# Kernel tuning notes

Hardware: AMD Instinct MI355X
Metric: run time of the kernel (lower is better)

Reference implementation:

```python
import jax, jax.numpy as jnp
import numpy as np

EMBED_DIM = 1024
TASK_BIAS_DIM = 128
BATCH = 4
SEQ = 2048


def setup_inputs() -> dict:
    key = jax.random.key(0)
    kq, kk, kv, kt, kw, kb = jax.random.split(key, 6)
    query = jax.random.normal(kq, (BATCH, SEQ, EMBED_DIM), dtype=jnp.float32)
    key_t = jax.random.normal(kk, (BATCH, SEQ, EMBED_DIM), dtype=jnp.float32)
    value = jax.random.normal(kv, (BATCH, SEQ, EMBED_DIM), dtype=jnp.float32)
    task_bias = jax.random.normal(kt, (BATCH, TASK_BIAS_DIM), dtype=jnp.float32)
    # task_bias_proj: Linear(task_bias_dim, 1) -> weight [1, task_bias_dim], bias [1]
    lim = 1.0 / np.sqrt(TASK_BIAS_DIM)
    W = jax.random.uniform(kw, (TASK_BIAS_DIM, 1), jnp.float32, -lim, lim)
    b = jax.random.uniform(kb, (1,), jnp.float32, -lim, lim)
    return {"query": query, "key": key_t, "value": value,
            "task_bias": task_bias, "W": W, "b": b}


def reference(query, key, value, task_bias, W, b):
    scale = EMBED_DIM ** 0.5
    # scores: [batch, seq, seq]
    scores = jnp.einsum('bqd,bkd->bqk', query, key) / scale
    # per-batch scalar gate from task bias: [batch, 1]
    gate = jax.nn.sigmoid(task_bias @ W + b)           # [batch, 1]
    scores = scores * gate[:, :, None]                 # broadcast [b,1,1]
    attention_weights = jax.nn.softmax(scores, axis=-1)
    output = jnp.einsum('bqk,bkd->bqd', attention_weights, value)
    return output, attention_weights
```

## Files before the change

kernel.cpp:

```cpp
#include <hip/hip_runtime.h>
#include <hip/hip_bf16.h>
#include <stdint.h>
#include <stddef.h>

#define B_  4
#define S_  2048
#define D_  1024
#define TB_ 128

typedef float v4f  __attribute__((ext_vector_type(4)));
typedef float v16f __attribute__((ext_vector_type(16)));
typedef short s16x4 __attribute__((ext_vector_type(4)));
typedef short s16x8 __attribute__((ext_vector_type(8)));

#define WAITV(n) asm volatile("s_waitcnt vmcnt(" #n ")" ::: "memory")

__device__ __forceinline__ unsigned short f2bf(float f) {
  union { float f; unsigned u; } x; x.f = f;
  unsigned u = x.u;
  unsigned r = (u + 0x7FFFu + ((u >> 16) & 1u)) >> 16;
  return (unsigned short)r;
}

__device__ __forceinline__ void gld16(const void* g, void* l) {
  __builtin_amdgcn_global_load_lds(
      (const __attribute__((address_space(1))) unsigned int*)g,
      (__attribute__((address_space(3))) unsigned int*)l, 16, 0, 0);
}

__device__ __forceinline__ void barrier_sync() {
  asm volatile("" ::: "memory");
  __builtin_amdgcn_s_barrier();
  asm volatile("" ::: "memory");
  __builtin_amdgcn_sched_barrier(0);
}

__global__ __launch_bounds__(256) void prep_kernel(
    const float* __restrict__ Q, const float* __restrict__ K,
    const float* __restrict__ V, const float* __restrict__ tb,
    const float* __restrict__ W, const float* __restrict__ bias,
    short* __restrict__ Qb, short* __restrict__ Kb,
    short* __restrict__ VT, float* __restrict__ gate) {
  __shared__ float tile[64][65];
  int bid = blockIdx.x;
  int t = threadIdx.x;
  if (bid < 16384) {
    const float* src = bid < 8192 ? Q : K;
    short* dst = bid < 8192 ? Qb : Kb;
    size_t g = (size_t)(bid & 8191) * 256 + t;
    v4f v = *(const v4f*)(src + g * 4);
    s16x4 o;
    o[0] = (short)f2bf(v[0]); o[1] = (short)f2bf(v[1]);
    o[2] = (short)f2bf(v[2]); o[3] = (short)f2bf(v[3]);
    *(s16x4*)(dst + g * 4) = o;
  } else if (bid < 18432) {
    int v = bid - 16384;
    int b = v >> 9;
    int rem = v & 511;
    int s0 = (rem & 31) * 64, d0 = (rem >> 5) * 64;
    int tc = t & 63, tr4 = t >> 6;
    const float* src = V + ((size_t)b * S_ + s0) * D_ + d0;
    #pragma unroll
    for (int p = 0; p < 16; ++p) {
      int r = p * 4 + tr4;
      tile[r][tc] = src[(size_t)r * D_ + tc];
    }
    __syncthreads();
    short* dst = VT + ((size_t)b * D_ + d0) * S_ + s0;
    #pragma unroll
    for (int p = 0; p < 16; ++p) {
      int r = p * 4 + tr4;
      dst[(size_t)r * S_ + tc] = (short)f2bf(tile[tc][r]);
    }
  } else {
    int b = t >> 6, l = t & 63;
    float s = tb[b * TB_ + l] * W[l] + tb[b * TB_ + 64 + l] * W[64 + l];
    #pragma unroll
    for (int off = 32; off > 0; off >>= 1) s += __shfl_down(s, off, 64);
    if (l == 0) gate[b] = 1.0f / (1.0f + __expf(-(s + bias[0])));
  }
}

template<int MFR, int NFR, int WNC, int BLOADS, int KT, int BROWS, int LDC,
         bool GATED>
__global__ __launch_bounds__(512, 2) void gemm_pipe(
    const short* __restrict__ Ag, const short* __restrict__ Bg,
    const float* __restrict__ gate, float* __restrict__ Cg) {
  extern __shared__ char lds[];
  constexpr int NT = KT / 64;
  constexpr int BN = WNC * NFR * 32;
  constexpr int ABYTES = 256 * 128;
  constexpr int BBYTES = BN * 128;
  constexpr int BUFB = ABYTES + BBYTES;

  int wg = blockIdx.x;
  int swz = (wg & 7) * 32 + (wg >> 3);
  int b = swz >> 6;
  int rem = swz & 63;
  int m0 = (rem >> 3) * 256;
  int n0 = (rem & 7) * BN;

  int tid = threadIdx.x;
  int w = tid >> 6, l = tid & 63;
  int wm = w / WNC, wn = w % WNC;
  int l7 = l & 7, col31 = l & 31, hi2 = l >> 5;

  const short* Ab = Ag + (size_t)b * S_ * KT + (size_t)m0 * KT;
  const short* Bb = Bg + (size_t)b * BROWS * KT + (size_t)n0 * KT;

  int srow8 = l >> 3;
  int schunk = ((l & 7) ^ srow8) * 8;

  v16f acc[MFR][NFR];
  #pragma unroll
  for (int m = 0; m < MFR; ++m)
    #pragma unroll
    for (int n = 0; n < NFR; ++n)
      #pragma unroll
      for (int j = 0; j < 16; ++j) acc[m][n][j] = 0.0f;

  auto stage = [&](int t, int buf) {
    char* La = lds + buf * BUFB;
    char* Lb = La + ABYTES;
    const short* As = Ab + (size_t)t * 64 + schunk;
    #pragma unroll
    for (int j = 0; j < 4; ++j) {
      int blk = w * 4 + j;
      gld16(As + (size_t)(blk * 8 + srow8) * KT, La + blk * 1024);
    }
    const short* Bs = Bb + (size_t)t * 64 + schunk;
    #pragma unroll
    for (int j = 0; j < BLOADS; ++j) {
      int blk = w * BLOADS + j;
      gld16(Bs + (size_t)(blk * 8 + srow8) * KT, Lb + blk * 1024);
    }
  };

  stage(0, 0);
  int cur = 0;
  for (int t = 0; t < NT; ++t) {
    if (t + 1 < NT) {
      stage(t + 1, cur ^ 1);
      if constexpr (BLOADS == 4) WAITV(8); else WAITV(6);
    } else {
      WAITV(0);
    }
    barrier_sync();
    const char* Abase = lds + cur * BUFB;
    const char* Bbase = Abase + ABYTES;
    #pragma unroll
    for (int ks = 0; ks < 4; ++ks) {
      int slot = ((ks * 2 + hi2) ^ l7) * 16;
      s16x8 bfr[NFR], af[MFR];
      #pragma unroll
      for (int n = 0; n < NFR; ++n)
        bfr[n] = *(const s16x8*)(Bbase +
                 (size_t)(wn * (NFR * 32) + n * 32 + col31) * 128 + slot);
      #pragma unroll
      for (int m = 0; m < MFR; ++m)
        af[m] = *(const s16x8*)(Abase +
                 (size_t)(wm * (MFR * 32) + m * 32 + col31) * 128 + slot);
      __builtin_amdgcn_s_setprio(1);
      #pragma unroll
      for (int m = 0; m < MFR; ++m)
        #pragma unroll
        for (int n = 0; n < NFR; ++n)
          acc[m][n] = __builtin_amdgcn_mfma_f32_32x32x16_bf16(
              af[m], bfr[n], acc[m][n], 0, 0, 0);
      __builtin_amdgcn_s_setprio(0);
    }
    barrier_sync();
    cur ^= 1;
  }

  float g = 1.0f;
  if constexpr (GATED) g = gate[b] * 0.03125f;
  float* Cb = Cg + (size_t)b * S_ * LDC +
              (size_t)(m0 + wm * (MFR * 32)) * LDC + n0 + wn * (NFR * 32);
  #pragma unroll
  for (int mf = 0; mf < MFR; ++mf)
    #pragma unroll
    for (int nf = 0; nf < NFR; ++nf) {
      int c = nf * 32 + col31;
      #pragma unroll
      for (int q = 0; q < 4; ++q)
        #pragma unroll
        for (int j = 0; j < 4; ++j) {
          int r = mf * 32 + q * 8 + 4 * hi2 + j;
          Cb[(size_t)r * LDC + c] = acc[mf][nf][q * 4 + j] * g;
        }
    }
}

__global__ __launch_bounds__(256) void softmax_kernel(
    float* __restrict__ attn, short* __restrict__ attnb) {
  size_t row = blockIdx.x;
  float* p = attn + row * S_;
  int t = threadIdx.x;
  v4f v0 = *(const v4f*)(p + t * 8);
  v4f v1 = *(const v4f*)(p + t * 8 + 4);
  float m = fmaxf(fmaxf(fmaxf(v0[0], v0[1]), fmaxf(v0[2], v0[3])),
                  fmaxf(fmaxf(v1[0], v1[1]), fmaxf(v1[2], v1[3])));
  #pragma unroll
  for (int off = 32; off > 0; off >>= 1) m = fmaxf(m, __shfl_xor(m, off, 64));
  __shared__ float rm[4], rs[4];
  if ((t & 63) == 0) rm[t >> 6] = m;
  __syncthreads();
  m = fmaxf(fmaxf(rm[0], rm[1]), fmaxf(rm[2], rm[3]));
  float e[8]; float sum = 0.0f;
  #pragma unroll
  for (int j = 0; j < 4; ++j) { e[j] = __expf(v0[j] - m); sum += e[j]; }
  #pragma unroll
  for (int j = 0; j < 4; ++j) { e[4 + j] = __expf(v1[j] - m); sum += e[4 + j]; }
  #pragma unroll
  for (int off = 32; off > 0; off >>= 1) sum += __shfl_xor(sum, off, 64);
  if ((t & 63) == 0) rs[t >> 6] = sum;
  __syncthreads();
  sum = rs[0] + rs[1] + rs[2] + rs[3];
  float inv = 1.0f / sum;
  #pragma unroll
  for (int j = 0; j < 4; ++j) v0[j] = e[j] * inv;
  #pragma unroll
  for (int j = 0; j < 4; ++j) v1[j] = e[4 + j] * inv;
  *(v4f*)(p + t * 8) = v0;
  *(v4f*)(p + t * 8 + 4) = v1;
  s16x8 ob;
  ob[0] = (short)f2bf(v0[0]); ob[1] = (short)f2bf(v0[1]);
  ob[2] = (short)f2bf(v0[2]); ob[3] = (short)f2bf(v0[3]);
  ob[4] = (short)f2bf(v1[0]); ob[5] = (short)f2bf(v1[1]);
  ob[6] = (short)f2bf(v1[2]); ob[7] = (short)f2bf(v1[3]);
  *(s16x8*)(attnb + row * S_ + t * 8) = ob;
}

extern "C" void kernel_launch(void* const* d_in, const int* in_sizes, int n_in,
                              void* d_out, int out_size, void* d_ws, size_t ws_size,
                              hipStream_t stream) {
  (void)in_sizes; (void)n_in; (void)out_size; (void)ws_size;
  const float* Q  = (const float*)d_in[0];
  const float* K  = (const float*)d_in[1];
  const float* V  = (const float*)d_in[2];
  const float* tb = (const float*)d_in[3];
  const float* W  = (const float*)d_in[4];
  const float* bias = (const float*)d_in[5];

  float* out  = (float*)d_out;
  float* attn = out + (size_t)B_ * S_ * D_;

  char* ws = (char*)d_ws;
  float* gate = (float*)ws;
  short* Qb = (short*)(ws + 256);
  short* Kb = Qb + (size_t)B_ * S_ * D_;
  short* VT = Kb + (size_t)B_ * S_ * D_;
  short* attnb = Qb;

  auto* qkf = gemm_pipe<4, 2, 4, 4, 1024, 2048, 2048, true>;
  auto* pvf = gemm_pipe<2, 2, 2, 2, 2048, 1024, 1024, false>;
  constexpr int QK_LDS = 2 * (256 + 256) * 64 * 2;
  constexpr int PV_LDS = 2 * (256 + 128) * 64 * 2;
  (void)hipFuncSetAttribute((const void*)qkf,
      hipFuncAttributeMaxDynamicSharedMemorySize, QK_LDS);
  (void)hipFuncSetAttribute((const void*)pvf,
      hipFuncAttributeMaxDynamicSharedMemorySize, PV_LDS);

  prep_kernel<<<18433, 256, 0, stream>>>(Q, K, V, tb, W, bias,
                                         Qb, Kb, VT, gate);
  qkf<<<256, 512, QK_LDS, stream>>>(Qb, Kb, gate, attn);
  softmax_kernel<<<8192, 256, 0, stream>>>(attn, attnb);
  pvf<<<256, 512, PV_LDS, stream>>>(attnb, VT, gate, out);
}
```

Measured before the change: 136.9 us.

## Shrink GEMM tiles to 128x128 with 256-thread blocks for more parallelism

Replaces the large-tile GEMM (256x256 or 256x128 per 512-thread block) with a 128x128 tile per 256-thread block where each wave computes a 64x64 sub-tile. This quadruples the grid for QK^T (1024 blocks) and doubles it for PV (512 blocks), aiming at better CU fill and wave-level parallelism on the 256-CU device. The cost is lower arithmetic intensity per tile: more global/LDS traffic per MFMA and fewer MFMAs per LDS fragment load.

```diff
diff --git a/kernel.cpp b/kernel.cpp
--- a/kernel.cpp
+++ b/kernel.cpp
@@ -81,41 +81,40 @@
   }
 }
 
-template<int MFR, int NFR, int WNC, int BLOADS, int KT, int BROWS, int LDC,
-         bool GATED>
-__global__ __launch_bounds__(512, 2) void gemm_pipe(
+template<int MTILES, int NTILES, int KT, int BROWS, int LDC, bool GATED>
+__global__ __launch_bounds__(256, 2) void gemm_tlp(
     const short* __restrict__ Ag, const short* __restrict__ Bg,
     const float* __restrict__ gate, float* __restrict__ Cg) {
   extern __shared__ char lds[];
   constexpr int NT = KT / 64;
-  constexpr int BN = WNC * NFR * 32;
-  constexpr int ABYTES = 256 * 128;
-  constexpr int BBYTES = BN * 128;
-  constexpr int BUFB = ABYTES + BBYTES;
+  constexpr int PB = MTILES * NTILES;
+  constexpr int CPX = (4 * PB) / 8;
+  constexpr int ABYTES = 128 * 128;
+  constexpr int BUFB = 2 * ABYTES;
 
   int wg = blockIdx.x;
-  int swz = (wg & 7) * 32 + (wg >> 3);
-  int b = swz >> 6;
-  int rem = swz & 63;
-  int m0 = (rem >> 3) * 256;
-  int n0 = (rem & 7) * BN;
+  int swz = (wg & 7) * CPX + (wg >> 3);
+  int b = swz / PB;
+  int rem = swz % PB;
+  int m0 = (rem / NTILES) * 128;
+  int n0 = (rem % NTILES) * 128;
 
   int tid = threadIdx.x;
   int w = tid >> 6, l = tid & 63;
-  int wm = w / WNC, wn = w % WNC;
+  int wm = w >> 1, wn = w & 1;
   int l7 = l & 7, col31 = l & 31, hi2 = l >> 5;
 
   const short* Ab = Ag + (size_t)b * S_ * KT + (size_t)m0 * KT;
   const short* Bb = Bg + (size_t)b * BROWS * KT + (size_t)n0 * KT;
 
-  int srow8 = l >> 3;
-  int schunk = ((l & 7) ^ srow8) * 8;
-
-  v16f acc[MFR][NFR];
-  #pragma unroll
-  for (int m = 0; m < MFR; ++m)
-    #pragma unroll
-    for (int n = 0; n < NFR; ++n)
+  int srow = tid >> 3;
+  int schunk = ((tid & 7) ^ (srow & 7)) * 8;
+
+  v16f acc[2][2];
+  #pragma unroll
+  for (int m = 0; m < 2; ++m)
+    #pragma unroll
+    for (int n = 0; n < 2; ++n)
       #pragma unroll
       for (int j = 0; j < 16; ++j) acc[m][n][j] = 0.0f;
 
@@ -123,17 +122,13 @@
     char* La = lds + buf * BUFB;
     char* Lb = La + ABYTES;
     const short* As = Ab + (size_t)t * 64 + schunk;
-    #pragma unroll
-    for (int j = 0; j < 4; ++j) {
-      int blk = w * 4 + j;
-      gld16(As + (size_t)(blk * 8 + srow8) * KT, La + blk * 1024);
-    }
     const short* Bs = Bb + (size_t)t * 64 + schunk;
     #pragma unroll
-    for (int j = 0; j < BLOADS; ++j) {
-      int blk = w * BLOADS + j;
-      gld16(Bs + (size_t)(blk * 8 + srow8) * KT, Lb + blk * 1024);
-    }
+    for (int j = 0; j < 4; ++j)
+      gld16(As + (size_t)(j * 32 + srow) * KT, La + j * 4096 + tid * 16);
+    #pragma unroll
+    for (int j = 0; j < 4; ++j)
+      gld16(Bs + (size_t)(j * 32 + srow) * KT, Lb + j * 4096 + tid * 16);
   };
 
   stage(0, 0);
@@ -141,7 +136,7 @@
   for (int t = 0; t < NT; ++t) {
     if (t + 1 < NT) {
       stage(t + 1, cur ^ 1);
-      if constexpr (BLOADS == 4) WAITV(8); else WAITV(6);
+      WAITV(8);
     } else {
       WAITV(0);
     }
@@ -151,20 +146,20 @@
     #pragma unroll
     for (int ks = 0; ks < 4; ++ks) {
       int slot = ((ks * 2 + hi2) ^ l7) * 16;
-      s16x8 bfr[NFR], af[MFR];
-      #pragma unroll
-      for (int n = 0; n < NFR; ++n)
+      s16x8 af[2], bfr[2];
+      #pragma unroll
+      for (int m = 0; m < 2; ++m)
+        af[m] = *(const s16x8*)(Abase +
+                 (size_t)(wm * 64 + m * 32 + col31) * 128 + slot);
+      #pragma unroll
+      for (int n = 0; n < 2; ++n)
         bfr[n] = *(const s16x8*)(Bbase +
-                 (size_t)(wn * (NFR * 32) + n * 32 + col31) * 128 + slot);
-      #pragma unroll
-      for (int m = 0; m < MFR; ++m)
-        af[m] = *(const s16x8*)(Abase +
-                 (size_t)(wm * (MFR * 32) + m * 32 + col31) * 128 + slot);
+                 (size_t)(wn * 64 + n * 32 + col31) * 128 + slot);
       __builtin_amdgcn_s_setprio(1);
       #pragma unroll
-      for (int m = 0; m < MFR; ++m)
+      for (int m = 0; m < 2; ++m)
         #pragma unroll
-        for (int n = 0; n < NFR; ++n)
+        for (int n = 0; n < 2; ++n)
           acc[m][n] = __builtin_amdgcn_mfma_f32_32x32x16_bf16(
               af[m], bfr[n], acc[m][n], 0, 0, 0);
       __builtin_amdgcn_s_setprio(0);
@@ -176,11 +171,11 @@
   float g = 1.0f;
   if constexpr (GATED) g = gate[b] * 0.03125f;
   float* Cb = Cg + (size_t)b * S_ * LDC +
-              (size_t)(m0 + wm * (MFR * 32)) * LDC + n0 + wn * (NFR * 32);
-  #pragma unroll
-  for (int mf = 0; mf < MFR; ++mf)
-    #pragma unroll
-    for (int nf = 0; nf < NFR; ++nf) {
+              (size_t)(m0 + wm * 64) * LDC + n0 + wn * 64;
+  #pragma unroll
+  for (int mf = 0; mf < 2; ++mf)
+    #pragma unroll
+    for (int nf = 0; nf < 2; ++nf) {
       int c = nf * 32 + col31;
       #pragma unroll
       for (int q = 0; q < 4; ++q)
@@ -253,18 +248,17 @@
   short* VT = Kb + (size_t)B_ * S_ * D_;
   short* attnb = Qb;
 
-  auto* qkf = gemm_pipe<4, 2, 4, 4, 1024, 2048, 2048, true>;
-  auto* pvf = gemm_pipe<2, 2, 2, 2, 2048, 1024, 1024, false>;
-  constexpr int QK_LDS = 2 * (256 + 256) * 64 * 2;
-  constexpr int PV_LDS = 2 * (256 + 128) * 64 * 2;
+  auto* qkf = gemm_tlp<16, 16, 1024, 2048, 2048, true>;
+  auto* pvf = gemm_tlp<16, 8, 2048, 1024, 1024, false>;
+  constexpr int G_LDS = 65536;
   (void)hipFuncSetAttribute((const void*)qkf,
-      hipFuncAttributeMaxDynamicSharedMemorySize, QK_LDS);
+      hipFuncAttributeMaxDynamicSharedMemorySize, G_LDS);
   (void)hipFuncSetAttribute((const void*)pvf,
-      hipFuncAttributeMaxDynamicSharedMemorySize, PV_LDS);
+      hipFuncAttributeMaxDynamicSharedMemorySize, G_LDS);
 
   prep_kernel<<<18433, 256, 0, stream>>>(Q, K, V, tb, W, bias,
                                          Qb, Kb, VT, gate);
-  qkf<<<256, 512, QK_LDS, stream>>>(Qb, Kb, gate, attn);
+  qkf<<<1024, 256, G_LDS, stream>>>(Qb, Kb, gate, attn);
   softmax_kernel<<<8192, 256, 0, stream>>>(attn, attnb);
-  pvf<<<256, 512, PV_LDS, stream>>>(attnb, VT, gate, out);
-}
+  pvf<<<512, 256, G_LDS, stream>>>(attnb, VT, gate, out);
+}
```

Result: slower. 141.7 us (+3.4%).

## Shrink GEMM workgroups and K-step to raise occupancy and workgroup count

Applied to the files above, without the earlier changes.

Restructures the bf16 MFMA GEMM kernel. Workgroups drop from 512 to 256 threads (4 waves in a 2x2 grid), output tiles shrink (256x128 for QK, 128x128 for PV), and the K-step per pipeline stage halves from 64 to 32 with a matching 4-chunk LDS swizzle. The grid doubles to 512 blocks and LDS per block drops, so more blocks can be resident per CU and the 256 CUs get more even coverage. The cost is more K iterations with a barrier each, less data reuse per tile, and more global traffic relative to the MFMA work.

```diff
diff --git a/kernel.cpp b/kernel.cpp
--- a/kernel.cpp
+++ b/kernel.cpp
@@ -81,35 +81,39 @@
   }
 }
 
-template<int MFR, int NFR, int WNC, int BLOADS, int KT, int BROWS, int LDC,
-         bool GATED>
-__global__ __launch_bounds__(512, 2) void gemm_pipe(
+template<int MTILES, int NTILES, int MFR, int NFR, int KT, int BROWS,
+         int LDC, bool GATED>
+__global__ __launch_bounds__(256, 2) void gemm_occ(
     const short* __restrict__ Ag, const short* __restrict__ Bg,
     const float* __restrict__ gate, float* __restrict__ Cg) {
   extern __shared__ char lds[];
-  constexpr int NT = KT / 64;
-  constexpr int BN = WNC * NFR * 32;
-  constexpr int ABYTES = 256 * 128;
-  constexpr int BBYTES = BN * 128;
-  constexpr int BUFB = ABYTES + BBYTES;
+  constexpr int BM = MFR * 64;
+  constexpr int BN = NFR * 64;
+  constexpr int ALOADS = BM / 64;
+  constexpr int BLOADS = BN / 64;
+  constexpr int NT = KT / 32;
+  constexpr int PB = MTILES * NTILES;
+  constexpr int CPX = (4 * PB) / 8;
+  constexpr int ABYTES = BM * 64;
+  constexpr int BUFB = ABYTES + BN * 64;
 
   int wg = blockIdx.x;
-  int swz = (wg & 7) * 32 + (wg >> 3);
-  int b = swz >> 6;
-  int rem = swz & 63;
-  int m0 = (rem >> 3) * 256;
-  int n0 = (rem & 7) * BN;
+  int swz = (wg & 7) * CPX + (wg >> 3);
+  int b = swz / PB;
+  int rem = swz % PB;
+  int m0 = (rem / NTILES) * BM;
+  int n0 = (rem % NTILES) * BN;
 
   int tid = threadIdx.x;
   int w = tid >> 6, l = tid & 63;
-  int wm = w / WNC, wn = w % WNC;
-  int l7 = l & 7, col31 = l & 31, hi2 = l >> 5;
+  int wm = w >> 1, wn = w & 1;
+  int col31 = l & 31, hi2 = l >> 5;
 
   const short* Ab = Ag + (size_t)b * S_ * KT + (size_t)m0 * KT;
   const short* Bb = Bg + (size_t)b * BROWS * KT + (size_t)n0 * KT;
 
-  int srow8 = l >> 3;
-  int schunk = ((l & 7) ^ srow8) * 8;
+  int srow = tid >> 2;
+  int schunk = ((tid & 3) ^ (srow & 3)) * 8;
 
   v16f acc[MFR][NFR];
   #pragma unroll
@@ -122,18 +126,14 @@
   auto stage = [&](int t, int buf) {
     char* La = lds + buf * BUFB;
     char* Lb = La + ABYTES;
-    const short* As = Ab + (size_t)t * 64 + schunk;
-    #pragma unroll
-    for (int j = 0; j < 4; ++j) {
-      int blk = w * 4 + j;
-      gld16(As + (size_t)(blk * 8 + srow8) * KT, La + blk * 1024);
-    }
-    const short* Bs = Bb + (size_t)t * 64 + schunk;
-    #pragma unroll
-    for (int j = 0; j < BLOADS; ++j) {
-      int blk = w * BLOADS + j;
-      gld16(Bs + (size_t)(blk * 8 + srow8) * KT, Lb + blk * 1024);
-    }
+    const short* As = Ab + (size_t)t * 32 + schunk;
+    const short* Bs = Bb + (size_t)t * 32 + schunk;
+    #pragma unroll
+    for (int j = 0; j < ALOADS; ++j)
+      gld16(As + (size_t)(j * 64 + srow) * KT, La + j * 4096 + tid * 16);
+    #pragma unroll
+    for (int j = 0; j < BLOADS; ++j)
+      gld16(Bs + (size_t)(j * 64 + srow) * KT, Lb + j * 4096 + tid * 16);
   };
 
   stage(0, 0);
@@ -141,7 +141,7 @@
   for (int t = 0; t < NT; ++t) {
     if (t + 1 < NT) {
       stage(t + 1, cur ^ 1);
-      if constexpr (BLOADS == 4) WAITV(8); else WAITV(6);
+      if constexpr (ALOADS + BLOADS == 6) WAITV(6); else WAITV(4);
     } else {
       WAITV(0);
     }
@@ -149,17 +149,17 @@
     const char* Abase = lds + cur * BUFB;
     const char* Bbase = Abase + ABYTES;
     #pragma unroll
-    for (int ks = 0; ks < 4; ++ks) {
-      int slot = ((ks * 2 + hi2) ^ l7) * 16;
-      s16x8 bfr[NFR], af[MFR];
+    for (int ks = 0; ks < 2; ++ks) {
+      int slot = ((ks * 2 + hi2) ^ (col31 & 3)) * 16;
+      s16x8 af[MFR], bfr[NFR];
+      #pragma unroll
+      for (int m = 0; m < MFR; ++m)
+        af[m] = *(const s16x8*)(Abase +
+                 (size_t)(wm * (MFR * 32) + m * 32 + col31) * 64 + slot);
       #pragma unroll
       for (int n = 0; n < NFR; ++n)
         bfr[n] = *(const s16x8*)(Bbase +
-                 (size_t)(wn * (NFR * 32) + n * 32 + col31) * 128 + slot);
-      #pragma unroll
-      for (int m = 0; m < MFR; ++m)
-        af[m] = *(const s16x8*)(Abase +
-                 (size_t)(wm * (MFR * 32) + m * 32 + col31) * 128 + slot);
+                 (size_t)(wn * (NFR * 32) + n * 32 + col31) * 64 + slot);
       __builtin_amdgcn_s_setprio(1);
       #pragma unroll
       for (int m = 0; m < MFR; ++m)
@@ -253,10 +253,10 @@
   short* VT = Kb + (size_t)B_ * S_ * D_;
   short* attnb = Qb;
 
-  auto* qkf = gemm_pipe<4, 2, 4, 4, 1024, 2048, 2048, true>;
-  auto* pvf = gemm_pipe<2, 2, 2, 2, 2048, 1024, 1024, false>;
-  constexpr int QK_LDS = 2 * (256 + 256) * 64 * 2;
-  constexpr int PV_LDS = 2 * (256 + 128) * 64 * 2;
+  auto* qkf = gemm_occ<8, 16, 4, 2, 1024, 2048, 2048, true>;
+  auto* pvf = gemm_occ<16, 8, 2, 2, 2048, 1024, 1024, false>;
+  constexpr int QK_LDS = 2 * (256 + 128) * 32 * 2;
+  constexpr int PV_LDS = 2 * (128 + 128) * 32 * 2;
   (void)hipFuncSetAttribute((const void*)qkf,
       hipFuncAttributeMaxDynamicSharedMemorySize, QK_LDS);
   (void)hipFuncSetAttribute((const void*)pvf,
@@ -264,7 +264,7 @@
 
   prep_kernel<<<18433, 256, 0, stream>>>(Q, K, V, tb, W, bias,
                                          Qb, Kb, VT, gate);
-  qkf<<<256, 512, QK_LDS, stream>>>(Qb, Kb, gate, attn);
+  qkf<<<512, 256, QK_LDS, stream>>>(Qb, Kb, gate, attn);
   softmax_kernel<<<8192, 256, 0, stream>>>(attn, attnb);
-  pvf<<<256, 512, PV_LDS, stream>>>(attnb, VT, gate, out);
-}
+  pvf<<<512, 256, PV_LDS, stream>>>(attnb, VT, gate, out);
+}
```

Result: slower. 146.7 us (+7.2%).

## Move fp32 attention-weight write from softmax into the PV GEMM epilogue

Applied to the files above, without the earlier changes.

The softmax kernel now writes only the bf16 probabilities. The PV GEMM kernel gains an epilogue in which each block converts 32 rows of the bf16 probabilities back to fp32 and writes them into the attention-weights output. The aim is to shorten the softmax pass and overlap the large fp32 store with the GEMM tail. In exchange, the returned attention weights are rounded to bf16 precision, and total memory traffic grows by an extra read of the bf16 matrix.

```diff
diff --git a/kernel.cpp b/kernel.cpp
--- a/kernel.cpp
+++ b/kernel.cpp
@@ -20,6 +20,12 @@
   unsigned u = x.u;
   unsigned r = (u + 0x7FFFu + ((u >> 16) & 1u)) >> 16;
   return (unsigned short)r;
+}
+
+__device__ __forceinline__ float bf2f(unsigned short s) {
+  union { unsigned u; float f; } x;
+  x.u = (unsigned)s << 16;
+  return x.f;
 }
 
 __device__ __forceinline__ void gld16(const void* g, void* l) {
@@ -82,10 +88,11 @@
 }
 
 template<int MFR, int NFR, int WNC, int BLOADS, int KT, int BROWS, int LDC,
-         bool GATED>
+         bool GATED, bool WATT>
 __global__ __launch_bounds__(512, 2) void gemm_pipe(
     const short* __restrict__ Ag, const short* __restrict__ Bg,
-    const float* __restrict__ gate, float* __restrict__ Cg) {
+    const float* __restrict__ gate, float* __restrict__ Cg,
+    const short* __restrict__ Pfull, float* __restrict__ attnOut) {
   extern __shared__ char lds[];
   constexpr int NT = KT / 64;
   constexpr int BN = WNC * NFR * 32;
@@ -109,7 +116,7 @@
   const short* Bb = Bg + (size_t)b * BROWS * KT + (size_t)n0 * KT;
 
   int srow8 = l >> 3;
-  int schunk = ((l & 7) ^ srow8) * 8;
+  int schunk = (l7 ^ srow8) * 8;
 
   v16f acc[MFR][NFR];
   #pragma unroll
@@ -190,12 +197,29 @@
           Cb[(size_t)r * LDC + c] = acc[mf][nf][q * 4 + j] * g;
         }
     }
+
+  if constexpr (WATT) {
+    int ni = rem & 7;
+    const short* Pb = Pfull + (size_t)b * S_ * S_;
+    float* Ob = attnOut + (size_t)b * S_ * S_;
+    #pragma unroll 4
+    for (int r = 0; r < 32; ++r) {
+      size_t off = (size_t)(m0 + ni * 32 + r) * S_ + tid * 4;
+      s16x4 pv = *(const s16x4*)(Pb + off);
+      v4f o;
+      o[0] = bf2f((unsigned short)pv[0]);
+      o[1] = bf2f((unsigned short)pv[1]);
+      o[2] = bf2f((unsigned short)pv[2]);
+      o[3] = bf2f((unsigned short)pv[3]);
+      *(v4f*)(Ob + off) = o;
+    }
+  }
 }
 
 __global__ __launch_bounds__(256) void softmax_kernel(
-    float* __restrict__ attn, short* __restrict__ attnb) {
+    const float* __restrict__ scores, short* __restrict__ attnb) {
   size_t row = blockIdx.x;
-  float* p = attn + row * S_;
+  const float* p = scores + row * S_;
   int t = threadIdx.x;
   v4f v0 = *(const v4f*)(p + t * 8);
   v4f v1 = *(const v4f*)(p + t * 8 + 4);
@@ -218,17 +242,9 @@
   __syncthreads();
   sum = rs[0] + rs[1] + rs[2] + rs[3];
   float inv = 1.0f / sum;
-  #pragma unroll
-  for (int j = 0; j < 4; ++j) v0[j] = e[j] * inv;
-  #pragma unroll
-  for (int j = 0; j < 4; ++j) v1[j] = e[4 + j] * inv;
-  *(v4f*)(p + t * 8) = v0;
-  *(v4f*)(p + t * 8 + 4) = v1;
   s16x8 ob;
-  ob[0] = (short)f2bf(v0[0]); ob[1] = (short)f2bf(v0[1]);
-  ob[2] = (short)f2bf(v0[2]); ob[3] = (short)f2bf(v0[3]);
-  ob[4] = (short)f2bf(v1[0]); ob[5] = (short)f2bf(v1[1]);
-  ob[6] = (short)f2bf(v1[2]); ob[7] = (short)f2bf(v1[3]);
+  #pragma unroll
+  for (int j = 0; j < 8; ++j) ob[j] = (short)f2bf(e[j] * inv);
   *(s16x8*)(attnb + row * S_ + t * 8) = ob;
 }
 
@@ -245,7 +261,6 @@
 
   float* out  = (float*)d_out;
   float* attn = out + (size_t)B_ * S_ * D_;
-
   char* ws = (char*)d_ws;
   float* gate = (float*)ws;
   short* Qb = (short*)(ws + 256);
@@ -253,8 +268,8 @@
   short* VT = Kb + (size_t)B_ * S_ * D_;
   short* attnb = Qb;
 
-  auto* qkf = gemm_pipe<4, 2, 4, 4, 1024, 2048, 2048, true>;
-  auto* pvf = gemm_pipe<2, 2, 2, 2, 2048, 1024, 1024, false>;
+  auto* qkf = gemm_pipe<4, 2, 4, 4, 1024, 2048, 2048, true, false>;
+  auto* pvf = gemm_pipe<2, 2, 2, 2, 2048, 1024, 1024, false, true>;
   constexpr int QK_LDS = 2 * (256 + 256) * 64 * 2;
   constexpr int PV_LDS = 2 * (256 + 128) * 64 * 2;
   (void)hipFuncSetAttribute((const void*)qkf,
@@ -264,7 +279,7 @@
 
   prep_kernel<<<18433, 256, 0, stream>>>(Q, K, V, tb, W, bias,
                                          Qb, Kb, VT, gate);
-  qkf<<<256, 512, QK_LDS, stream>>>(Qb, Kb, gate, attn);
+  qkf<<<256, 512, QK_LDS, stream>>>(Qb, Kb, gate, attn, nullptr, nullptr);
   softmax_kernel<<<8192, 256, 0, stream>>>(attn, attnb);
-  pvf<<<256, 512, PV_LDS, stream>>>(attnb, VT, gate, out);
-}
+  pvf<<<256, 512, PV_LDS, stream>>>(attnb, VT, gate, out, attnb, attn);
+}
```

After: 138.2 us. About the same (+0.9%).
